# Kernel optimization log

Hardware: AMD Instinct MI355X
Metric: run time of the kernel (lower is better)

Reference implementation:

```python
import jax, jax.numpy as jnp
import numpy as np

BN_EPS = 1e-5


def grid_sample_bilinear(img, grid):
    """Torch F.grid_sample, mode=bilinear, padding_mode=zeros, align_corners=False.
    img: (B, C, H, W); grid: (B, N, 2) in [-1, 1] -> (B, C, N)."""
    B, C, H, W = img.shape
    x = ((grid[..., 0] + 1.0) * W - 1.0) * 0.5  # (B, N) pixel coords
    y = ((grid[..., 1] + 1.0) * H - 1.0) * 0.5
    x0 = jnp.floor(x)
    y0 = jnp.floor(y)
    x1 = x0 + 1.0
    y1 = y0 + 1.0
    wx1 = x - x0
    wx0 = 1.0 - wx1
    wy1 = y - y0
    wy0 = 1.0 - wy1
    img_flat = img.reshape(B, C, H * W)

    def corner(xi, yi, w):
        valid = (xi >= 0) & (xi <= W - 1) & (yi >= 0) & (yi <= H - 1)
        xi_c = jnp.clip(xi, 0, W - 1).astype(jnp.int32)
        yi_c = jnp.clip(yi, 0, H - 1).astype(jnp.int32)
        idx = yi_c * W + xi_c  # (B, N)
        vals = jnp.take_along_axis(img_flat, idx[:, None, :], axis=2)  # (B, C, N)
        return vals * (w * valid.astype(img.dtype))[:, None, :]

    return (corner(x0, y0, wx0 * wy0) + corner(x1, y0, wx1 * wy0)
            + corner(x0, y1, wx0 * wy1) + corner(x1, y1, wx1 * wy1))


def conv1x1(x, w, b):
    # x: (B, Cin, N), w: (Cout, Cin), b: (Cout,)
    return jnp.einsum('oi,bin->bon', w, x) + b[None, :, None]


def batchnorm1d_train(x, gamma, beta):
    # training-mode BN over (batch, length) per channel, biased variance
    mean = jnp.mean(x, axis=(0, 2), keepdims=True)
    var = jnp.mean((x - mean) ** 2, axis=(0, 2), keepdims=True)
    xn = (x - mean) * jax.lax.rsqrt(var + BN_EPS)
    return xn * gamma[None, :, None] + beta[None, :, None]


def setup_inputs() -> dict:
    key = jax.random.key(0)
    ks = jax.random.split(key, 12)
    B, N, CI, CP, H, W, R = 4, 16384, 256, 256, 64, 160, 4
    Cin = CI + CP
    Cb = CP // R

    def glorot(k, shape):
        fan_in = shape[1]
        return jax.random.normal(k, shape, dtype=jnp.float32) * (1.0 / np.sqrt(fan_in))

    return {
        'pts_img': jax.random.uniform(ks[0], (B, N, 2), dtype=jnp.float32, minval=-1.0, maxval=1.0),
        'img_feats': jax.random.normal(ks[1], (B, CI, H, W), dtype=jnp.float32),
        'pts_feats': jax.random.normal(ks[2], (B, CP, N), dtype=jnp.float32),
        'fusion_w': glorot(ks[3], (CP, Cin)),
        'fusion_b': jax.random.normal(ks[4], (CP,), dtype=jnp.float32) * 0.01,
        'bn_gamma': jnp.ones((CP,), dtype=jnp.float32),
        'bn_beta': jnp.zeros((CP,), dtype=jnp.float32),
        'ca1_w': glorot(ks[5], (Cb, CP)),
        'ca1_b': jax.random.normal(ks[6], (Cb,), dtype=jnp.float32) * 0.01,
        'ca2_w': glorot(ks[7], (CP, Cb)),
        'ca2_b': jax.random.normal(ks[8], (CP,), dtype=jnp.float32) * 0.01,
        'sa_w': glorot(ks[9], (Cb, CP)),
        'sa_b': jax.random.normal(ks[10], (Cb,), dtype=jnp.float32) * 0.01,
    }


def reference(pts_img, img_feats, pts_feats, fusion_w, fusion_b, bn_gamma, bn_beta,
              ca1_w, ca1_b, ca2_w, ca2_b, sa_w, sa_b):
    # grid_sample gather: (B, C_I, N)
    pts_wise_img_feats = grid_sample_bilinear(img_feats, pts_img)
    fusion = jnp.concatenate([pts_wise_img_feats, pts_feats], axis=1)  # (B, C_I+C_P, N)
    # fusion MLP: conv1x1 + BN + ReLU
    fusion = jax.nn.relu(batchnorm1d_train(conv1x1(fusion, fusion_w, fusion_b), bn_gamma, bn_beta))
    # spatial attention: max over channels of bottleneck conv, sigmoid gate
    spatial = jax.nn.sigmoid(jnp.max(conv1x1(fusion, sa_w, sa_b), axis=1, keepdims=True))
    fusion = spatial * fusion
    # channel attention: bottleneck MLP, global max-pool over points, sigmoid gate
    ca = conv1x1(jax.nn.relu(conv1x1(fusion, ca1_w, ca1_b)), ca2_w, ca2_b)  # (B, C_P, N)
    channel = jax.nn.sigmoid(jnp.max(ca, axis=2, keepdims=True))  # (B, C_P, 1)
    return channel * fusion
```

## Files before the change

### kernel.cpp

```cpp
#include <hip/hip_runtime.h>
#include <stdint.h>


typedef __attribute__((ext_vector_type(8))) short bf16x8;
typedef __attribute__((ext_vector_type(4))) float f32x4;

#define B_ 4
#define N_ 16384
#define H_ 64
#define W_ 160
#define HW_ (H_ * W_)
#define K_ 512

__device__ __forceinline__ float bf2f(unsigned short u) {
    union { unsigned int i; float f; } c; c.i = ((unsigned int)u) << 16; return c.f;
}
__device__ __forceinline__ unsigned short f2bf(float f) {
    union { float f; unsigned int i; } c; c.f = f;
    unsigned int u = c.i;
    return (unsigned short)((u + 0x7FFFu + ((u >> 16) & 1u)) >> 16);
}
__device__ __forceinline__ unsigned int fkey(float f) {
    union { float f; unsigned int u; int i; } c; c.f = f;
    return (c.i < 0) ? ~c.u : (c.u | 0x80000000u);
}
__device__ __forceinline__ float funkey(unsigned int k) {
    union { unsigned int u; float f; } c;
    c.u = (k & 0x80000000u) ? (k & 0x7FFFFFFFu) : ~k;
    return c.f;
}

__device__ __forceinline__ void async_copy16(void* lds, const void* g) {
#if defined(__has_builtin) && __has_builtin(__builtin_amdgcn_global_load_lds)
    __builtin_amdgcn_global_load_lds(
        (const __attribute__((address_space(1))) unsigned int*)g,
        (__attribute__((address_space(3))) unsigned int*)lds, 16, 0, 0);
#else
    *(uint4*)lds = *(const uint4*)g;
#endif
}

__global__ void k_wcvt(const float* __restrict__ fw, const float* __restrict__ saw,
                       const float* __restrict__ c1w, const float* __restrict__ c2w,
                       unsigned short* WfB, unsigned short* saB,
                       unsigned short* ca1B, unsigned short* ca2B,
                       float* buckets, unsigned int* camax) {
    int t = threadIdx.x;
    if (blockIdx.x == 0) {
        for (int i = t; i < 16 * 512; i += 256) buckets[i] = 0.f;
        for (int i = t; i < 8 * 1024; i += 256) camax[i] = 0u;
    }
    int i = blockIdx.x * 256 + t;
    if (i < 131072) WfB[i] = f2bf(fw[i]);
    else if (i < 147456) saB[i - 131072] = f2bf(saw[i - 131072]);
    else if (i < 163840) ca1B[i - 147456] = f2bf(c1w[i - 147456]);
    else if (i < 180224) ca2B[i - 163840] = f2bf(c2w[i - 163840]);
}

__global__ __launch_bounds__(256) void k_imgt(const float* __restrict__ img,
                                              unsigned short* __restrict__ imgT) {
    __shared__ __align__(16) unsigned short tile[64 * 72];
    int t = threadIdx.x;
    int hw0 = blockIdx.x * 64, c0 = blockIdx.y * 64, b = blockIdx.z;
    const float* src = img + ((size_t)b * 256 + c0) * HW_ + hw0;
    int sub = (t & 15) * 4, grp = t >> 4;
#pragma unroll
    for (int it = 0; it < 4; ++it) {
        int cl = grp + it * 16;
        float4 v = *(const float4*)(src + (size_t)cl * HW_ + sub);
        ushort4 o;
        o.x = f2bf(v.x); o.y = f2bf(v.y); o.z = f2bf(v.z); o.w = f2bf(v.w);
        *(ushort4*)(tile + cl * 72 + sub) = o;
    }
    __syncthreads();
    unsigned short* dst = imgT + ((size_t)b * HW_ + hw0) * 256 + c0;
#pragma unroll
    for (int it = 0; it < 4; ++it) {
        int hwl = grp + it * 16;
        ushort4 o;
        o.x = tile[(sub + 0) * 72 + hwl];
        o.y = tile[(sub + 1) * 72 + hwl];
        o.z = tile[(sub + 2) * 72 + hwl];
        o.w = tile[(sub + 3) * 72 + hwl];
        *(ushort4*)(dst + (size_t)hwl * 256 + sub) = o;
    }
}

__global__ __launch_bounds__(256) void k_ptst(const float* __restrict__ pts,
                                              unsigned short* __restrict__ XT) {
    __shared__ __align__(16) unsigned short tile[64 * 72];
    int t = threadIdx.x;
    int n0 = blockIdx.x * 64, c0 = blockIdx.y * 64, b = blockIdx.z;
    const float* src = pts + ((size_t)b * 256 + c0) * N_ + n0;
    int sub = (t & 15) * 4, grp = t >> 4;
#pragma unroll
    for (int it = 0; it < 4; ++it) {
        int cl = grp + it * 16;
        float4 v = *(const float4*)(src + (size_t)cl * N_ + sub);
        ushort4 o;
        o.x = f2bf(v.x); o.y = f2bf(v.y); o.z = f2bf(v.z); o.w = f2bf(v.w);
        *(ushort4*)(tile + cl * 72 + sub) = o;
    }
    __syncthreads();
    unsigned short* dst = XT + ((size_t)b * N_ + n0) * K_ + 256 + c0;
#pragma unroll
    for (int it = 0; it < 4; ++it) {
        int nl = grp + it * 16;
        ushort4 o;
        o.x = tile[(sub + 0) * 72 + nl];
        o.y = tile[(sub + 1) * 72 + nl];
        o.z = tile[(sub + 2) * 72 + nl];
        o.w = tile[(sub + 3) * 72 + nl];
        *(ushort4*)(dst + (size_t)nl * K_ + sub) = o;
    }
}

__global__ __launch_bounds__(256) void k_gather(const float* __restrict__ pim,
                                                const unsigned short* __restrict__ imgT,
                                                unsigned short* __restrict__ XT) {
    int t = threadIdx.x;
    int w = t >> 6, lane = t & 63;
    int p0 = blockIdx.x * 16 + w * 4;
    int c = lane * 4;
    for (int pp = 0; pp < 4; ++pp) {
        int p = p0 + pp;
        int b = p >> 14;
        float gx = pim[(size_t)p * 2 + 0];
        float gy = pim[(size_t)p * 2 + 1];
        float x = (gx + 1.0f) * (0.5f * W_) - 0.5f;
        float y = (gy + 1.0f) * (0.5f * H_) - 0.5f;
        float xf = floorf(x), yf = floorf(y);
        float wx1 = x - xf, wx0 = 1.0f - wx1;
        float wy1 = y - yf, wy0 = 1.0f - wy1;
        int x0 = (int)xf, y0 = (int)yf;
        int x1 = x0 + 1, y1 = y0 + 1;
        float vx0 = (x0 >= 0 && x0 < W_) ? 1.f : 0.f;
        float vx1 = (x1 >= 0 && x1 < W_) ? 1.f : 0.f;
        float vy0 = (y0 >= 0 && y0 < H_) ? 1.f : 0.f;
        float vy1 = (y1 >= 0 && y1 < H_) ? 1.f : 0.f;
        int cx0 = min(max(x0, 0), W_ - 1), cx1 = min(max(x1, 0), W_ - 1);
        int cy0 = min(max(y0, 0), H_ - 1), cy1 = min(max(y1, 0), H_ - 1);
        float w00 = wx0 * wy0 * vx0 * vy0;
        float w10 = wx1 * wy0 * vx1 * vy0;
        float w01 = wx0 * wy1 * vx0 * vy1;
        float w11 = wx1 * wy1 * vx1 * vy1;
        const unsigned short* base = imgT + (size_t)b * HW_ * 256;
        ushort4 a00 = *(const ushort4*)(base + ((size_t)cy0 * W_ + cx0) * 256 + c);
        ushort4 a10 = *(const ushort4*)(base + ((size_t)cy0 * W_ + cx1) * 256 + c);
        ushort4 a01 = *(const ushort4*)(base + ((size_t)cy1 * W_ + cx0) * 256 + c);
        ushort4 a11 = *(const ushort4*)(base + ((size_t)cy1 * W_ + cx1) * 256 + c);
        ushort4 o;
        o.x = f2bf(w00 * bf2f(a00.x) + w10 * bf2f(a10.x) + w01 * bf2f(a01.x) + w11 * bf2f(a11.x));
        o.y = f2bf(w00 * bf2f(a00.y) + w10 * bf2f(a10.y) + w01 * bf2f(a01.y) + w11 * bf2f(a11.y));
        o.z = f2bf(w00 * bf2f(a00.z) + w10 * bf2f(a10.z) + w01 * bf2f(a01.z) + w11 * bf2f(a11.z));
        o.w = f2bf(w00 * bf2f(a00.w) + w10 * bf2f(a10.w) + w01 * bf2f(a01.w) + w11 * bf2f(a11.w));
        *(ushort4*)(XT + (size_t)p * K_ + c) = o;
    }
}

__global__ __launch_bounds__(256, 2) void k_gemm1(const unsigned short* __restrict__ WfB,
                                                  const unsigned short* __restrict__ XT,
                                                  const float* __restrict__ fb,
                                                  unsigned short* __restrict__ Y,
                                                  float* __restrict__ buckets) {
    __shared__ __align__(16) unsigned short At[128 * 32];
    __shared__ __align__(16) unsigned short Bt[128 * 32];
    __shared__ float biasS[128];
    __shared__ float redS[2][128], redQ[2][128];
    int t = threadIdx.x;
    int n0 = blockIdx.x * 128, m0 = blockIdx.y * 128, b = blockIdx.z;
    if (t < 128) biasS[t] = fb[m0 + t];
    const unsigned short* Xb = XT + (size_t)b * N_ * K_;
    int w = t >> 6, lane = t & 63, quad = lane >> 4, l15 = lane & 15;
    int wm = w >> 1, wn = w & 1;
    int srow = lane >> 2, scol = (lane & 3) * 8;
    const f32x4 fzero = {0.f, 0.f, 0.f, 0.f};
    f32x4 acc[4][4];
#pragma unroll
    for (int i = 0; i < 4; ++i)
#pragma unroll
        for (int j = 0; j < 4; ++j) acc[i][j] = fzero;
    for (int kt = 0; kt < 16; ++kt) {
        int k0 = kt * 32;
        __syncthreads();
#pragma unroll
        for (int cch = 0; cch < 2; ++cch) {
            int chunk = w * 2 + cch;
            int row = chunk * 16 + srow;
            async_copy16(At + chunk * 512 + lane * 8,
                         WfB + (size_t)(m0 + row) * K_ + k0 + scol);
            async_copy16(Bt + chunk * 512 + lane * 8,
                         Xb + (size_t)(n0 + row) * K_ + k0 + scol);
        }
        __syncthreads();
        bf16x8 af[4], bv[4];
#pragma unroll
        for (int i = 0; i < 4; ++i) {
            af[i] = *(const bf16x8*)(At + (wm * 64 + i * 16 + l15) * 32 + quad * 8);
            bv[i] = *(const bf16x8*)(Bt + (wn * 64 + i * 16 + l15) * 32 + quad * 8);
        }
#pragma unroll
        for (int i = 0; i < 4; ++i)
#pragma unroll
            for (int j = 0; j < 4; ++j)
                acc[i][j] = __builtin_amdgcn_mfma_f32_16x16x32_bf16(af[i], bv[j], acc[i][j], 0, 0, 0);
    }
    size_t Yb = (size_t)b * N_ * 256;
#pragma unroll
    for (int i = 0; i < 4; ++i) {
        int mloc = wm * 64 + i * 16 + quad * 4;
        float b0 = biasS[mloc + 0], b1 = biasS[mloc + 1];
        float b2 = biasS[mloc + 2], b3 = biasS[mloc + 3];
        float bb[4] = {b0, b1, b2, b3};
#pragma unroll
        for (int j = 0; j < 4; ++j) {
            int n = n0 + wn * 64 + j * 16 + l15;
            ushort4 o;
            o.x = f2bf(acc[i][j][0] + b0);
            o.y = f2bf(acc[i][j][1] + b1);
            o.z = f2bf(acc[i][j][2] + b2);
            o.w = f2bf(acc[i][j][3] + b3);
            *(ushort4*)(Y + Yb + (size_t)n * 256 + m0 + mloc) = o;
        }
#pragma unroll
        for (int r = 0; r < 4; ++r) {
            float s = 0.f, q = 0.f;
#pragma unroll
            for (int j = 0; j < 4; ++j) {
                float y = acc[i][j][r] + bb[r];
                s += y;
                q += y * y;
            }
#pragma unroll
            for (int d = 1; d < 16; d <<= 1) {
                s += __shfl_xor(s, d, 64);
                q += __shfl_xor(q, d, 64);
            }
            if (l15 == 0) {
                redS[wn][mloc + r] = s;
                redQ[wn][mloc + r] = q;
            }
        }
    }
    __syncthreads();
    if (t < 128) {
        float* bk = buckets + (size_t)(blockIdx.x & 15) * 512;
        atomicAdd(bk + m0 + t, redS[0][t] + redS[1][t]);
        atomicAdd(bk + 256 + m0 + t, redQ[0][t] + redQ[1][t]);
    }
}

__global__ __launch_bounds__(256, 1) void k_gate(unsigned short* __restrict__ F,
                                                 const float* __restrict__ buckets,
                                                 const float* __restrict__ gamma,
                                                 const float* __restrict__ beta,
                                                 const unsigned short* __restrict__ saB,
                                                 const float* __restrict__ sab,
                                                 const unsigned short* __restrict__ c1B,
                                                 const float* __restrict__ c1b,
                                                 const unsigned short* __restrict__ c2B,
                                                 unsigned int* __restrict__ camax) {
    __shared__ __align__(16) unsigned short Ft[64 * 264];
    __shared__ __align__(16) unsigned short WSb[256 * 72];
    __shared__ __align__(16) unsigned short Ht[64 * 72];
    __shared__ float scS[256], shS[256];
    __shared__ float biasS[64];
    __shared__ float sp[64];
    int t = threadIdx.x;
    size_t pts0 = (size_t)blockIdx.x * 64;
    int b = (int)(pts0 >> 14);
    int w = t >> 6, lane = t & 63, quad = lane >> 4, l15 = lane & 15;

    {
        float s = 0.f, q = 0.f;
#pragma unroll
        for (int bk = 0; bk < 16; ++bk) {
            s += buckets[bk * 512 + t];
            q += buckets[bk * 512 + 256 + t];
        }
        const float inv = 1.0f / (float)(B_ * N_);
        float mean = s * inv;
        float var = q * inv - mean * mean;
        float sc = gamma[t] * rsqrtf(var + 1e-5f);
        scS[t] = sc;
        shS[t] = beta[t] - mean * sc;
    }
    for (int idx = t * 8; idx < 64 * 256; idx += 2048) {
        int r = idx >> 8, c = idx & 255;
        *(uint4*)(WSb + r * 264 + c) = *(const uint4*)(saB + r * 256 + c);
    }
    if (t < 64) biasS[t] = sab[t];
    __syncthreads();

    for (int idx = t * 8; idx < 64 * 256; idx += 2048) {
        int r = idx >> 8, c = idx & 255;
        uint4 v = *(const uint4*)(F + (pts0 + r) * 256 + c);
        unsigned short* us = (unsigned short*)&v;
#pragma unroll
        for (int e = 0; e < 8; ++e) {
            float f = bf2f(us[e]) * scS[c + e] + shS[c + e];
            us[e] = f2bf(fmaxf(f, 0.f));
        }
        *(uint4*)(Ft + r * 264 + c) = v;
    }
    __syncthreads();

    {
        const f32x4 fzero = {0.f, 0.f, 0.f, 0.f};
        f32x4 acc[4] = {fzero, fzero, fzero, fzero};
        for (int kt = 0; kt < 8; ++kt) {
            int k0 = kt * 32;
            bf16x8 af = *(const bf16x8*)(Ft + (w * 16 + l15) * 264 + k0 + quad * 8);
#pragma unroll
            for (int jt = 0; jt < 4; ++jt) {
                bf16x8 bv = *(const bf16x8*)(WSb + (jt * 16 + l15) * 264 + k0 + quad * 8);
                acc[jt] = __builtin_amdgcn_mfma_f32_16x16x32_bf16(af, bv, acc[jt], 0, 0, 0);
            }
        }
        float sb[4];
#pragma unroll
        for (int jt = 0; jt < 4; ++jt) sb[jt] = biasS[jt * 16 + l15];
#pragma unroll
        for (int r = 0; r < 4; ++r) {
            float v = acc[0][r] + sb[0];
            v = fmaxf(v, acc[1][r] + sb[1]);
            v = fmaxf(v, acc[2][r] + sb[2]);
            v = fmaxf(v, acc[3][r] + sb[3]);
#pragma unroll
            for (int d = 1; d < 16; d <<= 1) v = fmaxf(v, __shfl_xor(v, d, 64));
            if (l15 == 0) sp[w * 16 + quad * 4 + r] = 1.0f / (1.0f + __expf(-v));
        }
    }
    __syncthreads();

    for (int idx = t * 8; idx < 64 * 256; idx += 2048) {
        int r = idx >> 8, c = idx & 255;
        float s = sp[r];
        uint4 v = *(uint4*)(Ft + r * 264 + c);
        unsigned short* us = (unsigned short*)&v;
#pragma unroll
        for (int e = 0; e < 8; ++e) us[e] = f2bf(bf2f(us[e]) * s);
        *(uint4*)(Ft + r * 264 + c) = v;
        *(uint4*)(F + (pts0 + r) * 256 + c) = v;
    }
    for (int idx = t * 8; idx < 64 * 256; idx += 2048) {
        int r = idx >> 8, c = idx & 255;
        *(uint4*)(WSb + r * 264 + c) = *(const uint4*)(c1B + r * 256 + c);
    }
    if (t < 64) biasS[t] = c1b[t];
    __syncthreads();

    {
        const f32x4 fzero = {0.f, 0.f, 0.f, 0.f};
        f32x4 acc[4] = {fzero, fzero, fzero, fzero};
        for (int kt = 0; kt < 8; ++kt) {
            int k0 = kt * 32;
            bf16x8 af = *(const bf16x8*)(Ft + (w * 16 + l15) * 264 + k0 + quad * 8);
#pragma unroll
            for (int jt = 0; jt < 4; ++jt) {
                bf16x8 bv = *(const bf16x8*)(WSb + (jt * 16 + l15) * 264 + k0 + quad * 8);
                acc[jt] = __builtin_amdgcn_mfma_f32_16x16x32_bf16(af, bv, acc[jt], 0, 0, 0);
            }
        }
#pragma unroll
        for (int jt = 0; jt < 4; ++jt) {
            float bb = biasS[jt * 16 + l15];
#pragma unroll
            for (int r = 0; r < 4; ++r) {
                int pt = w * 16 + quad * 4 + r;
                Ht[pt * 72 + jt * 16 + l15] = f2bf(fmaxf(acc[jt][r] + bb, 0.f));
            }
        }
    }
    __syncthreads();

    for (int idx = t * 8; idx < 256 * 64; idx += 2048) {
        int r = idx >> 6, c = idx & 63;
        *(uint4*)(WSb + r * 72 + c) = *(const uint4*)(c2B + r * 64 + c);
    }
    __syncthreads();

    {
        const f32x4 fzero = {0.f, 0.f, 0.f, 0.f};
        f32x4 acc[4][4];
#pragma unroll
        for (int i = 0; i < 4; ++i)
#pragma unroll
            for (int mt = 0; mt < 4; ++mt) acc[i][mt] = fzero;
#pragma unroll
        for (int kk = 0; kk < 2; ++kk) {
            bf16x8 af[4], bv[4];
#pragma unroll
            for (int i = 0; i < 4; ++i)
                af[i] = *(const bf16x8*)(Ht + (i * 16 + l15) * 72 + kk * 32 + quad * 8);
#pragma unroll
            for (int mt = 0; mt < 4; ++mt)
                bv[mt] = *(const bf16x8*)(WSb + (w * 64 + mt * 16 + l15) * 72 + kk * 32 + quad * 8);
#pragma unroll
            for (int i = 0; i < 4; ++i)
#pragma unroll
                for (int mt = 0; mt < 4; ++mt)
                    acc[i][mt] = __builtin_amdgcn_mfma_f32_16x16x32_bf16(af[i], bv[mt], acc[i][mt], 0, 0, 0);
        }
        unsigned int* cam = camax + (size_t)(blockIdx.x & 7) * 1024 + b * 256;
#pragma unroll
        for (int mt = 0; mt < 4; ++mt) {
            float v = acc[0][mt][0];
#pragma unroll
            for (int i = 0; i < 4; ++i)
#pragma unroll
                for (int r = 0; r < 4; ++r) v = fmaxf(v, acc[i][mt][r]);
            v = fmaxf(v, __shfl_xor(v, 16, 64));
            v = fmaxf(v, __shfl_xor(v, 32, 64));
            if (quad == 0) atomicMax(cam + w * 64 + mt * 16 + l15, fkey(v));
        }
    }
}

__global__ __launch_bounds__(256) void k_out(const unsigned short* __restrict__ F,
                                             const unsigned int* __restrict__ camax,
                                             const float* __restrict__ c2b,
                                             float* __restrict__ out) {
    __shared__ __align__(16) unsigned short tile[64 * 72];
    __shared__ float ch[64];
    int t = threadIdx.x;
    int n0 = blockIdx.x * 64, m0 = blockIdx.y * 64, b = blockIdx.z;
    if (t < 64) {
        int m = m0 + t;
        unsigned int k = 0u;
#pragma unroll
        for (int bk = 0; bk < 8; ++bk) k = max(k, camax[bk * 1024 + b * 256 + m]);
        float v = funkey(k) + c2b[m];
        ch[t] = 1.0f / (1.0f + __expf(-v));
    }
    int sub = (t & 15) * 4, grp = t >> 4;
    const unsigned short* src = F + (size_t)b * N_ * 256;
#pragma unroll
    for (int it = 0; it < 4; ++it) {
        int nl = grp + it * 16;
        ushort4 v = *(const ushort4*)(src + (size_t)(n0 + nl) * 256 + m0 + sub);
        *(ushort4*)(tile + nl * 72 + sub) = v;
    }
    __syncthreads();
    float* dst = out + ((size_t)b * 256 + m0) * N_ + n0;
#pragma unroll
    for (int it = 0; it < 4; ++it) {
        int ml = grp + it * 16;
        float g = ch[ml];
        float4 o;
        o.x = bf2f(tile[(sub + 0) * 72 + ml]) * g;
        o.y = bf2f(tile[(sub + 1) * 72 + ml]) * g;
        o.z = bf2f(tile[(sub + 2) * 72 + ml]) * g;
        o.w = bf2f(tile[(sub + 3) * 72 + ml]) * g;
        *(float4*)(dst + (size_t)ml * N_ + sub) = o;
    }
}

extern "C" void kernel_launch(void* const* d_in, const int* in_sizes, int n_in,
                              void* d_out, int out_size, void* d_ws, size_t ws_size,
                              hipStream_t stream) {
    (void)in_sizes; (void)n_in; (void)out_size; (void)ws_size;
    const float* pts_img = (const float*)d_in[0];
    const float* img     = (const float*)d_in[1];
    const float* pts     = (const float*)d_in[2];
    const float* fw      = (const float*)d_in[3];
    const float* fbias   = (const float*)d_in[4];
    const float* gamma   = (const float*)d_in[5];
    const float* beta    = (const float*)d_in[6];
    const float* c1w     = (const float*)d_in[7];
    const float* c1b     = (const float*)d_in[8];
    const float* c2w     = (const float*)d_in[9];
    const float* c2b     = (const float*)d_in[10];
    const float* saw     = (const float*)d_in[11];
    const float* sab     = (const float*)d_in[12];
    float* out = (float*)d_out;

    char* ws = (char*)d_ws;
    unsigned short* XT   = (unsigned short*)(ws);
    unsigned short* imgT = (unsigned short*)(ws + 67108864);
    unsigned short* Y    = (unsigned short*)(ws + 67108864);
    unsigned short* WfB  = (unsigned short*)(ws + 100663296);
    unsigned short* saB  = (unsigned short*)(ws + 100925440);
    unsigned short* ca1B = (unsigned short*)(ws + 100958208);
    unsigned short* ca2B = (unsigned short*)(ws + 100990976);
    float* buckets       = (float*)(ws + 101023744);
    unsigned int* camax  = (unsigned int*)(ws + 101056512);

    k_wcvt<<<704, 256, 0, stream>>>(fw, saw, c1w, c2w, WfB, saB, ca1B, ca2B, buckets, camax);
    k_imgt<<<dim3(160, 4, 4), 256, 0, stream>>>(img, imgT);
    k_gather<<<4096, 256, 0, stream>>>(pts_img, imgT, XT);
    k_ptst<<<dim3(256, 4, 4), 256, 0, stream>>>(pts, XT);
    k_gemm1<<<dim3(128, 2, 4), 256, 0, stream>>>(WfB, XT, fbias, Y, buckets);
    k_gate<<<1024, 256, 0, stream>>>(Y, buckets, gamma, beta, saB, sab, ca1B, c1b, ca2B, camax);
    k_out<<<dim3(256, 4, 4), 256, 0, stream>>>(Y, camax, c2b, out);
}
```

Baseline: 295.4 us.

## Merge gather, point transpose and weight conversion; read gate weights from global

Three small preprocessing kernels (weight conversion and buffer zeroing, bilinear gather, point-feature transpose) are combined into one launch that dispatches on block index. This removes two launches and lets the independent pieces overlap. In k_gate the shared-memory staging of the attention weights is dropped, so MFMA B operands are loaded straight from global/L2. That frees LDS so launch bounds can rise to three blocks per CU, and BN scale/shift are hoisted into registers. The risk is that repeated global weight loads inside the MFMA loops cost more latency than the LDS copies they replace.

```diff
diff --git a/kernel.cpp b/kernel.cpp
--- a/kernel.cpp
+++ b/kernel.cpp
@@ -40,23 +40,6 @@
 #endif
 }
 
-__global__ void k_wcvt(const float* __restrict__ fw, const float* __restrict__ saw,
-                       const float* __restrict__ c1w, const float* __restrict__ c2w,
-                       unsigned short* WfB, unsigned short* saB,
-                       unsigned short* ca1B, unsigned short* ca2B,
-                       float* buckets, unsigned int* camax) {
-    int t = threadIdx.x;
-    if (blockIdx.x == 0) {
-        for (int i = t; i < 16 * 512; i += 256) buckets[i] = 0.f;
-        for (int i = t; i < 8 * 1024; i += 256) camax[i] = 0u;
-    }
-    int i = blockIdx.x * 256 + t;
-    if (i < 131072) WfB[i] = f2bf(fw[i]);
-    else if (i < 147456) saB[i - 131072] = f2bf(saw[i - 131072]);
-    else if (i < 163840) ca1B[i - 147456] = f2bf(c1w[i - 147456]);
-    else if (i < 180224) ca2B[i - 163840] = f2bf(c2w[i - 163840]);
-}
-
 __global__ __launch_bounds__(256) void k_imgt(const float* __restrict__ img,
                                               unsigned short* __restrict__ imgT) {
     __shared__ __align__(16) unsigned short tile[64 * 72];
@@ -86,75 +69,94 @@
     }
 }
 
-__global__ __launch_bounds__(256) void k_ptst(const float* __restrict__ pts,
-                                              unsigned short* __restrict__ XT) {
+__global__ __launch_bounds__(256) void k_xt(const float* __restrict__ pim,
+                                            const unsigned short* __restrict__ imgT,
+                                            const float* __restrict__ pts,
+                                            unsigned short* __restrict__ XT,
+                                            const float* __restrict__ fw,
+                                            const float* __restrict__ saw,
+                                            const float* __restrict__ c1w,
+                                            const float* __restrict__ c2w,
+                                            unsigned short* WfB, unsigned short* saB,
+                                            unsigned short* ca1B, unsigned short* ca2B,
+                                            float* buckets, unsigned int* camax) {
     __shared__ __align__(16) unsigned short tile[64 * 72];
     int t = threadIdx.x;
-    int n0 = blockIdx.x * 64, c0 = blockIdx.y * 64, b = blockIdx.z;
-    const float* src = pts + ((size_t)b * 256 + c0) * N_ + n0;
-    int sub = (t & 15) * 4, grp = t >> 4;
-#pragma unroll
-    for (int it = 0; it < 4; ++it) {
-        int cl = grp + it * 16;
-        float4 v = *(const float4*)(src + (size_t)cl * N_ + sub);
-        ushort4 o;
-        o.x = f2bf(v.x); o.y = f2bf(v.y); o.z = f2bf(v.z); o.w = f2bf(v.w);
-        *(ushort4*)(tile + cl * 72 + sub) = o;
-    }
-    __syncthreads();
-    unsigned short* dst = XT + ((size_t)b * N_ + n0) * K_ + 256 + c0;
-#pragma unroll
-    for (int it = 0; it < 4; ++it) {
-        int nl = grp + it * 16;
-        ushort4 o;
-        o.x = tile[(sub + 0) * 72 + nl];
-        o.y = tile[(sub + 1) * 72 + nl];
-        o.z = tile[(sub + 2) * 72 + nl];
-        o.w = tile[(sub + 3) * 72 + nl];
-        *(ushort4*)(dst + (size_t)nl * K_ + sub) = o;
-    }
-}
-
-__global__ __launch_bounds__(256) void k_gather(const float* __restrict__ pim,
-                                                const unsigned short* __restrict__ imgT,
-                                                unsigned short* __restrict__ XT) {
-    int t = threadIdx.x;
-    int w = t >> 6, lane = t & 63;
-    int p0 = blockIdx.x * 16 + w * 4;
-    int c = lane * 4;
-    for (int pp = 0; pp < 4; ++pp) {
-        int p = p0 + pp;
-        int b = p >> 14;
-        float gx = pim[(size_t)p * 2 + 0];
-        float gy = pim[(size_t)p * 2 + 1];
-        float x = (gx + 1.0f) * (0.5f * W_) - 0.5f;
-        float y = (gy + 1.0f) * (0.5f * H_) - 0.5f;
-        float xf = floorf(x), yf = floorf(y);
-        float wx1 = x - xf, wx0 = 1.0f - wx1;
-        float wy1 = y - yf, wy0 = 1.0f - wy1;
-        int x0 = (int)xf, y0 = (int)yf;
-        int x1 = x0 + 1, y1 = y0 + 1;
-        float vx0 = (x0 >= 0 && x0 < W_) ? 1.f : 0.f;
-        float vx1 = (x1 >= 0 && x1 < W_) ? 1.f : 0.f;
-        float vy0 = (y0 >= 0 && y0 < H_) ? 1.f : 0.f;
-        float vy1 = (y1 >= 0 && y1 < H_) ? 1.f : 0.f;
-        int cx0 = min(max(x0, 0), W_ - 1), cx1 = min(max(x1, 0), W_ - 1);
-        int cy0 = min(max(y0, 0), H_ - 1), cy1 = min(max(y1, 0), H_ - 1);
-        float w00 = wx0 * wy0 * vx0 * vy0;
-        float w10 = wx1 * wy0 * vx1 * vy0;
-        float w01 = wx0 * wy1 * vx0 * vy1;
-        float w11 = wx1 * wy1 * vx1 * vy1;
-        const unsigned short* base = imgT + (size_t)b * HW_ * 256;
-        ushort4 a00 = *(const ushort4*)(base + ((size_t)cy0 * W_ + cx0) * 256 + c);
-        ushort4 a10 = *(const ushort4*)(base + ((size_t)cy0 * W_ + cx1) * 256 + c);
-        ushort4 a01 = *(const ushort4*)(base + ((size_t)cy1 * W_ + cx0) * 256 + c);
-        ushort4 a11 = *(const ushort4*)(base + ((size_t)cy1 * W_ + cx1) * 256 + c);
-        ushort4 o;
-        o.x = f2bf(w00 * bf2f(a00.x) + w10 * bf2f(a10.x) + w01 * bf2f(a01.x) + w11 * bf2f(a11.x));
-        o.y = f2bf(w00 * bf2f(a00.y) + w10 * bf2f(a10.y) + w01 * bf2f(a01.y) + w11 * bf2f(a11.y));
-        o.z = f2bf(w00 * bf2f(a00.z) + w10 * bf2f(a10.z) + w01 * bf2f(a01.z) + w11 * bf2f(a11.z));
-        o.w = f2bf(w00 * bf2f(a00.w) + w10 * bf2f(a10.w) + w01 * bf2f(a01.w) + w11 * bf2f(a11.w));
-        *(ushort4*)(XT + (size_t)p * K_ + c) = o;
+    int bx = blockIdx.x;
+    if (bx < 4096) {
+        int w = t >> 6, lane = t & 63;
+        int p0 = bx * 16 + w * 4;
+        int c = lane * 4;
+        for (int pp = 0; pp < 4; ++pp) {
+            int p = p0 + pp;
+            int b = p >> 14;
+            float gx = pim[(size_t)p * 2 + 0];
+            float gy = pim[(size_t)p * 2 + 1];
+            float x = (gx + 1.0f) * (0.5f * W_) - 0.5f;
+            float y = (gy + 1.0f) * (0.5f * H_) - 0.5f;
+            float xf = floorf(x), yf = floorf(y);
+            float wx1 = x - xf, wx0 = 1.0f - wx1;
+            float wy1 = y - yf, wy0 = 1.0f - wy1;
+            int x0 = (int)xf, y0 = (int)yf;
+            int x1 = x0 + 1, y1 = y0 + 1;
+            float vx0 = (x0 >= 0 && x0 < W_) ? 1.f : 0.f;
+            float vx1 = (x1 >= 0 && x1 < W_) ? 1.f : 0.f;
+            float vy0 = (y0 >= 0 && y0 < H_) ? 1.f : 0.f;
+            float vy1 = (y1 >= 0 && y1 < H_) ? 1.f : 0.f;
+            int cx0 = min(max(x0, 0), W_ - 1), cx1 = min(max(x1, 0), W_ - 1);
+            int cy0 = min(max(y0, 0), H_ - 1), cy1 = min(max(y1, 0), H_ - 1);
+            float w00 = wx0 * wy0 * vx0 * vy0;
+            float w10 = wx1 * wy0 * vx1 * vy0;
+            float w01 = wx0 * wy1 * vx0 * vy1;
+            float w11 = wx1 * wy1 * vx1 * vy1;
+            const unsigned short* base = imgT + (size_t)b * HW_ * 256;
+            ushort4 a00 = *(const ushort4*)(base + ((size_t)cy0 * W_ + cx0) * 256 + c);
+            ushort4 a10 = *(const ushort4*)(base + ((size_t)cy0 * W_ + cx1) * 256 + c);
+            ushort4 a01 = *(const ushort4*)(base + ((size_t)cy1 * W_ + cx0) * 256 + c);
+            ushort4 a11 = *(const ushort4*)(base + ((size_t)cy1 * W_ + cx1) * 256 + c);
+            ushort4 o;
+            o.x = f2bf(w00 * bf2f(a00.x) + w10 * bf2f(a10.x) + w01 * bf2f(a01.x) + w11 * bf2f(a11.x));
+            o.y = f2bf(w00 * bf2f(a00.y) + w10 * bf2f(a10.y) + w01 * bf2f(a01.y) + w11 * bf2f(a11.y));
+            o.z = f2bf(w00 * bf2f(a00.z) + w10 * bf2f(a10.z) + w01 * bf2f(a01.z) + w11 * bf2f(a11.z));
+            o.w = f2bf(w00 * bf2f(a00.w) + w10 * bf2f(a10.w) + w01 * bf2f(a01.w) + w11 * bf2f(a11.w));
+            *(ushort4*)(XT + (size_t)p * K_ + c) = o;
+        }
+    } else if (bx < 8192) {
+        int j = bx - 4096;
+        int n0 = (j & 255) * 64, c0 = ((j >> 8) & 3) * 64, b = j >> 10;
+        const float* src = pts + ((size_t)b * 256 + c0) * N_ + n0;
+        int sub = (t & 15) * 4, grp = t >> 4;
+#pragma unroll
+        for (int it = 0; it < 4; ++it) {
+            int cl = grp + it * 16;
+            float4 v = *(const float4*)(src + (size_t)cl * N_ + sub);
+            ushort4 o;
+            o.x = f2bf(v.x); o.y = f2bf(v.y); o.z = f2bf(v.z); o.w = f2bf(v.w);
+            *(ushort4*)(tile + cl * 72 + sub) = o;
+        }
+        __syncthreads();
+        unsigned short* dst = XT + ((size_t)b * N_ + n0) * K_ + 256 + c0;
+#pragma unroll
+        for (int it = 0; it < 4; ++it) {
+            int nl = grp + it * 16;
+            ushort4 o;
+            o.x = tile[(sub + 0) * 72 + nl];
+            o.y = tile[(sub + 1) * 72 + nl];
+            o.z = tile[(sub + 2) * 72 + nl];
+            o.w = tile[(sub + 3) * 72 + nl];
+            *(ushort4*)(dst + (size_t)nl * K_ + sub) = o;
+        }
+    } else {
+        int j = bx - 8192;
+        if (j == 0) {
+            for (int i = t; i < 16 * 512; i += 256) buckets[i] = 0.f;
+            for (int i = t; i < 8 * 1024; i += 256) camax[i] = 0u;
+        }
+        int i = j * 256 + t;
+        if (i < 131072) WfB[i] = f2bf(fw[i]);
+        else if (i < 147456) saB[i - 131072] = f2bf(saw[i - 131072]);
+        else if (i < 163840) ca1B[i - 147456] = f2bf(c1w[i - 147456]);
+        else if (i < 180224) ca2B[i - 163840] = f2bf(c2w[i - 163840]);
     }
 }
 
@@ -250,7 +252,7 @@
     }
 }
 
-__global__ __launch_bounds__(256, 1) void k_gate(unsigned short* __restrict__ F,
+__global__ __launch_bounds__(256, 3) void k_gate(unsigned short* __restrict__ F,
                                                  const float* __restrict__ buckets,
                                                  const float* __restrict__ gamma,
                                                  const float* __restrict__ beta,
@@ -261,10 +263,8 @@
                                                  const unsigned short* __restrict__ c2B,
                                                  unsigned int* __restrict__ camax) {
     __shared__ __align__(16) unsigned short Ft[64 * 264];
-    __shared__ __align__(16) unsigned short WSb[256 * 72];
     __shared__ __align__(16) unsigned short Ht[64 * 72];
     __shared__ float scS[256], shS[256];
-    __shared__ float biasS[64];
     __shared__ float sp[64];
     int t = threadIdx.x;
     size_t pts0 = (size_t)blockIdx.x * 64;
@@ -285,23 +285,22 @@
         scS[t] = sc;
         shS[t] = beta[t] - mean * sc;
     }
+    __syncthreads();
+
+    int cc = (t * 8) & 255;
+    float scr[8], shr[8];
+#pragma unroll
+    for (int e = 0; e < 8; ++e) { scr[e] = scS[cc + e]; shr[e] = shS[cc + e]; }
     for (int idx = t * 8; idx < 64 * 256; idx += 2048) {
-        int r = idx >> 8, c = idx & 255;
-        *(uint4*)(WSb + r * 264 + c) = *(const uint4*)(saB + r * 256 + c);
-    }
-    if (t < 64) biasS[t] = sab[t];
-    __syncthreads();
-
-    for (int idx = t * 8; idx < 64 * 256; idx += 2048) {
-        int r = idx >> 8, c = idx & 255;
-        uint4 v = *(const uint4*)(F + (pts0 + r) * 256 + c);
+        int r = idx >> 8;
+        uint4 v = *(const uint4*)(F + (pts0 + r) * 256 + cc);
         unsigned short* us = (unsigned short*)&v;
 #pragma unroll
         for (int e = 0; e < 8; ++e) {
-            float f = bf2f(us[e]) * scS[c + e] + shS[c + e];
+            float f = bf2f(us[e]) * scr[e] + shr[e];
             us[e] = f2bf(fmaxf(f, 0.f));
         }
-        *(uint4*)(Ft + r * 264 + c) = v;
+        *(uint4*)(Ft + r * 264 + cc) = v;
     }
     __syncthreads();
 
@@ -313,13 +312,13 @@
             bf16x8 af = *(const bf16x8*)(Ft + (w * 16 + l15) * 264 + k0 + quad * 8);
 #pragma unroll
             for (int jt = 0; jt < 4; ++jt) {
-                bf16x8 bv = *(const bf16x8*)(WSb + (jt * 16 + l15) * 264 + k0 + quad * 8);
+                bf16x8 bv = *(const bf16x8*)(saB + (size_t)(jt * 16 + l15) * 256 + k0 + quad * 8);
                 acc[jt] = __builtin_amdgcn_mfma_f32_16x16x32_bf16(af, bv, acc[jt], 0, 0, 0);
             }
         }
         float sb[4];
 #pragma unroll
-        for (int jt = 0; jt < 4; ++jt) sb[jt] = biasS[jt * 16 + l15];
+        for (int jt = 0; jt < 4; ++jt) sb[jt] = sab[jt * 16 + l15];
 #pragma unroll
         for (int r = 0; r < 4; ++r) {
             float v = acc[0][r] + sb[0];
@@ -334,20 +333,15 @@
     __syncthreads();
 
     for (int idx = t * 8; idx < 64 * 256; idx += 2048) {
-        int r = idx >> 8, c = idx & 255;
+        int r = idx >> 8;
         float s = sp[r];
-        uint4 v = *(uint4*)(Ft + r * 264 + c);
+        uint4 v = *(uint4*)(Ft + r * 264 + cc);
         unsigned short* us = (unsigned short*)&v;
 #pragma unroll
         for (int e = 0; e < 8; ++e) us[e] = f2bf(bf2f(us[e]) * s);
-        *(uint4*)(Ft + r * 264 + c) = v;
-        *(uint4*)(F + (pts0 + r) * 256 + c) = v;
-    }
-    for (int idx = t * 8; idx < 64 * 256; idx += 2048) {
-        int r = idx >> 8, c = idx & 255;
-        *(uint4*)(WSb + r * 264 + c) = *(const uint4*)(c1B + r * 256 + c);
-    }
-    if (t < 64) biasS[t] = c1b[t];
+        *(uint4*)(Ft + r * 264 + cc) = v;
+        *(uint4*)(F + (pts0 + r) * 256 + cc) = v;
+    }
     __syncthreads();
 
     {
@@ -358,13 +352,13 @@
             bf16x8 af = *(const bf16x8*)(Ft + (w * 16 + l15) * 264 + k0 + quad * 8);
 #pragma unroll
             for (int jt = 0; jt < 4; ++jt) {
-                bf16x8 bv = *(const bf16x8*)(WSb + (jt * 16 + l15) * 264 + k0 + quad * 8);
+                bf16x8 bv = *(const bf16x8*)(c1B + (size_t)(jt * 16 + l15) * 256 + k0 + quad * 8);
                 acc[jt] = __builtin_amdgcn_mfma_f32_16x16x32_bf16(af, bv, acc[jt], 0, 0, 0);
             }
         }
 #pragma unroll
         for (int jt = 0; jt < 4; ++jt) {
-            float bb = biasS[jt * 16 + l15];
+            float bb = c1b[jt * 16 + l15];
 #pragma unroll
             for (int r = 0; r < 4; ++r) {
                 int pt = w * 16 + quad * 4 + r;
@@ -374,12 +368,6 @@
     }
     __syncthreads();
 
-    for (int idx = t * 8; idx < 256 * 64; idx += 2048) {
-        int r = idx >> 6, c = idx & 63;
-        *(uint4*)(WSb + r * 72 + c) = *(const uint4*)(c2B + r * 64 + c);
-    }
-    __syncthreads();
-
     {
         const f32x4 fzero = {0.f, 0.f, 0.f, 0.f};
         f32x4 acc[4][4];
@@ -395,7 +383,7 @@
                 af[i] = *(const bf16x8*)(Ht + (i * 16 + l15) * 72 + kk * 32 + quad * 8);
 #pragma unroll
             for (int mt = 0; mt < 4; ++mt)
-                bv[mt] = *(const bf16x8*)(WSb + (w * 64 + mt * 16 + l15) * 72 + kk * 32 + quad * 8);
+                bv[mt] = *(const bf16x8*)(c2B + (size_t)(w * 64 + mt * 16 + l15) * 64 + kk * 32 + quad * 8);
 #pragma unroll
             for (int i = 0; i < 4; ++i)
 #pragma unroll
@@ -486,10 +474,9 @@
     float* buckets       = (float*)(ws + 101023744);
     unsigned int* camax  = (unsigned int*)(ws + 101056512);
 
-    k_wcvt<<<704, 256, 0, stream>>>(fw, saw, c1w, c2w, WfB, saB, ca1B, ca2B, buckets, camax);
     k_imgt<<<dim3(160, 4, 4), 256, 0, stream>>>(img, imgT);
-    k_gather<<<4096, 256, 0, stream>>>(pts_img, imgT, XT);
-    k_ptst<<<dim3(256, 4, 4), 256, 0, stream>>>(pts, XT);
+    k_xt<<<8896, 256, 0, stream>>>(pts_img, imgT, pts, XT, fw, saw, c1w, c2w,
+                                   WfB, saB, ca1B, ca2B, buckets, camax);
     k_gemm1<<<dim3(128, 2, 4), 256, 0, stream>>>(WfB, XT, fbias, Y, buckets);
     k_gate<<<1024, 256, 0, stream>>>(Y, buckets, gamma, beta, saB, sab, ca1B, c1b, ca2B, camax);
     k_out<<<dim3(256, 4, 4), 256, 0, stream>>>(Y, camax, c2b, out);
```

Result: no change. 291.8 us (-1.2%).
